# Kernel tuning notes

Measured on AMD Instinct MI355X. Metric: run time of the kernel, lower is better.

The kernel has to match this reference:

```python
import jax, jax.numpy as jnp
import numpy as np

EMB = 256
T = 32          # block_size (hardcoded causal mask length)
HEAD = 128      # total head_size
NH = 8          # n_heads
DH = HEAD // NH # 16 per-head size
B = 4096
EPS = 1e-5


def _ln(x, g, b):
    mu = jnp.mean(x, -1, keepdims=True)
    var = jnp.var(x, -1, keepdims=True)
    return (x - mu) * jax.lax.rsqrt(var + EPS) * g + b


def setup_inputs() -> dict:
    key = jax.random.key(0)
    ks = jax.random.split(key, 12)
    s_in = 1.0 / np.sqrt(EMB)
    s_h = 1.0 / np.sqrt(HEAD)
    s_ff = 1.0 / np.sqrt(4 * EMB)
    return {
        "X": jax.random.normal(ks[0], (B, T, EMB), jnp.float32),
        "ln_g": jnp.ones((EMB,), jnp.float32),
        "ln_b": jnp.zeros((EMB,), jnp.float32),
        # per-head Q/K/V projections packed: [EMB, HEAD] == concat of NH [EMB, DH] heads
        "Wq": jax.random.uniform(ks[1], (EMB, HEAD), jnp.float32, -s_in, s_in),
        "bq": jax.random.uniform(ks[2], (HEAD,), jnp.float32, -s_in, s_in),
        "Wk": jax.random.uniform(ks[3], (EMB, HEAD), jnp.float32, -s_in, s_in),
        "bk": jax.random.uniform(ks[4], (HEAD,), jnp.float32, -s_in, s_in),
        "Wv": jax.random.uniform(ks[5], (EMB, HEAD), jnp.float32, -s_in, s_in),
        "bv": jax.random.uniform(ks[6], (HEAD,), jnp.float32, -s_in, s_in),
        "Wo": jax.random.uniform(ks[7], (HEAD, EMB), jnp.float32, -s_h, s_h),
        "bo": jax.random.uniform(ks[8], (EMB,), jnp.float32, -s_h, s_h),
        "W1": jax.random.uniform(ks[9], (EMB, 4 * EMB), jnp.float32, -s_in, s_in),
        "b1": jax.random.uniform(ks[10], (4 * EMB,), jnp.float32, -s_in, s_in),
        "W2": jax.random.uniform(ks[11], (4 * EMB, EMB), jnp.float32, -s_ff, s_ff),
        "b2": jax.random.uniform(jax.random.fold_in(key, 99), (EMB,), jnp.float32, -s_ff, s_ff),
    }


def reference(X, ln_g, ln_b, Wq, bq, Wk, bk, Wv, bv, Wo, bo, W1, b1, W2, b2):
    h = _ln(X, ln_g, ln_b)                              # [B,T,E]
    # packed QKV, split into heads: [B,T,NH,DH]
    Q = (h @ Wq + bq).reshape(B, T, NH, DH)
    K = (h @ Wk + bk).reshape(B, T, NH, DH)
    V = (h @ Wv + bv).reshape(B, T, NH, DH)
    scores = jnp.einsum("bqhd,bkhd->bhqk", Q, K)        # [B,NH,T,T]
    mask = jnp.tril(jnp.ones((T, T), bool))
    # original: masked_fill(-inf) then divide by sqrt(dh); -inf unchanged
    scores = jnp.where(mask, scores / np.sqrt(DH), -jnp.inf)
    attn = jax.nn.softmax(scores, -1)
    ctx = jnp.einsum("bhqk,bkhd->bqhd", attn, V).reshape(B, T, HEAD)
    X = ctx @ Wo + bo + X                               # residual 1
    h2 = _ln(X, ln_g, ln_b)                             # shared LN params
    out = jax.nn.relu(h2 @ W1 + b1) @ W2 + b2 + X       # residual 2
    return out
```

## Files before the change

### kernel.cpp

```cpp
#include <hip/hip_runtime.h>
#include <math.h>

typedef __attribute__((ext_vector_type(8))) __bf16 bf16x8;
typedef __attribute__((ext_vector_type(8))) unsigned short u16x8;
typedef __attribute__((ext_vector_type(4))) unsigned short u16x4;
typedef __attribute__((ext_vector_type(4))) float f32x4;

namespace {
constexpr int EMB = 256;
constexpr int HD  = 128;
constexpr int FF  = 1024;
constexpr float EPSV = 1e-5f;

constexpr int WS_QKV = 0;
constexpr int WS_O   = 98304;
constexpr int WS_1   = 131072;
constexpr int WS_2   = 393216;

__device__ __forceinline__ unsigned short f32_to_bf16(float f) {
    return __builtin_bit_cast(unsigned short, (__bf16)f);
}
__device__ __forceinline__ float bf16_to_f32(unsigned short h) {
    return __builtin_bit_cast(float, ((unsigned int)h) << 16);
}
__device__ __forceinline__ f32x4 mfma16(u16x8 a, u16x8 b, f32x4 c) {
    return __builtin_amdgcn_mfma_f32_16x16x32_bf16(
        __builtin_bit_cast(bf16x8, a), __builtin_bit_cast(bf16x8, b), c, 0, 0, 0);
}
__device__ __forceinline__ int swzB(int row) { return (row & 7) << 4; }

__device__ __forceinline__ u16x8 ldsA256(const unsigned short* base, int row, int k0) {
    int byte = (row * 256 + k0 * 2) ^ swzB(row);
    return *(const u16x8*)((const char*)base + byte);
}
__device__ __forceinline__ u16x8 ldsA512(const unsigned short* base, int row, int k0) {
    int byte = (row * 512 + k0 * 2) ^ swzB(row);
    return *(const u16x8*)((const char*)base + byte);
}
__device__ __forceinline__ u16x8 ldgF(const unsigned short* base, int frag, int lane) {
    return *(const u16x8*)(base + ((size_t)frag * 64 + lane) * 8);
}
}

__global__ __launch_bounds__(256) void wconv(
    const float* __restrict__ Wq, const float* __restrict__ Wk, const float* __restrict__ Wv,
    const float* __restrict__ Wo, const float* __restrict__ W1, const float* __restrict__ W2,
    unsigned short* __restrict__ ws) {
    int e = blockIdx.x * 256 + threadIdx.x;
    int j, lane, kk, nt, n, k;
    float v;
    if (e < WS_O) {
        int t = e; j = t & 7; lane = (t >> 3) & 63; int r2 = t >> 9;
        kk = r2 & 7; nt = r2 >> 3;
        n = nt * 16 + (lane & 15); k = kk * 32 + (lane >> 4) * 8 + j;
        const float* W = (n < 128) ? Wq : ((n < 256) ? Wk : Wv);
        v = W[k * HD + (n & 127)];
    } else if (e < WS_1) {
        int t = e - WS_O; j = t & 7; lane = (t >> 3) & 63; int r2 = t >> 9;
        kk = r2 & 3; nt = r2 >> 2;
        n = nt * 16 + (lane & 15); k = kk * 32 + (lane >> 4) * 8 + j;
        v = Wo[k * EMB + n];
    } else if (e < WS_2) {
        int t = e - WS_1; j = t & 7; lane = (t >> 3) & 63; int r2 = t >> 9;
        kk = r2 & 7; nt = r2 >> 3;
        n = nt * 16 + (lane & 15); k = kk * 32 + (lane >> 4) * 8 + j;
        v = W1[k * FF + n];
    } else {
        int t = e - WS_2; j = t & 7; lane = (t >> 3) & 63; int r2 = t >> 9;
        kk = r2 & 31; nt = r2 >> 5;
        n = nt * 16 + (lane & 15); k = kk * 32 + (lane >> 4) * 8 + j;
        v = W2[k * EMB + n];
    }
    ws[e] = f32_to_bf16(v);
}

__global__ __launch_bounds__(256, 2) void attn_part(
    const float* __restrict__ X, const float* __restrict__ ln_g, const float* __restrict__ ln_b,
    const float* __restrict__ bq, const float* __restrict__ bk, const float* __restrict__ bv,
    const float* __restrict__ bo, const unsigned short* __restrict__ ws,
    float* __restrict__ x1out) {
    __shared__ __attribute__((aligned(16))) char smem[40960];
    unsigned short* hb = (unsigned short*)smem;
    unsigned short* Qb = (unsigned short*)(smem + 16384);
    char* Kc           = smem + 24576;
    char* Vc           = smem + 32768;

    const unsigned short* WTqkv = ws + WS_QKV;
    const unsigned short* WTo   = ws + WS_O;

    const int tid  = threadIdx.x;
    const int wv   = tid >> 6;
    const int mh   = wv & 1;
    const int nh   = wv >> 1;
    const int lane = tid & 63;
    const int lr   = lane & 15;
    const int lh   = lane >> 4;
    const int row0 = blockIdx.x * 32;
    const f32x4 Z  = {0.f, 0.f, 0.f, 0.f};

    {
        const int r = tid >> 3, sub = tid & 7;
        const float* xr = X + (size_t)(row0 + r) * EMB;
        float4 vv[8];
        float s = 0.f, ss = 0.f;
        #pragma unroll
        for (int j = 0; j < 8; ++j) {
            float4 v = *(const float4*)&xr[sub * 4 + j * 32];
            vv[j] = v;
            s  += (v.x + v.y) + (v.z + v.w);
            ss += (v.x * v.x + v.y * v.y) + (v.z * v.z + v.w * v.w);
        }
        #pragma unroll
        for (int w = 1; w < 8; w <<= 1) { s += __shfl_xor(s, w, 64); ss += __shfl_xor(ss, w, 64); }
        float mu  = s * (1.f / EMB);
        float inv = rsqrtf(fmaxf(ss * (1.f / EMB) - mu * mu, 0.f) + EPSV);
        #pragma unroll
        for (int j = 0; j < 8; ++j) {
            int c = sub * 4 + j * 32;
            float4 v = vv[j];
            float4 g4 = *(const float4*)&ln_g[c];
            float4 b4 = *(const float4*)&ln_b[c];
            u16x4 pk;
            pk[0] = f32_to_bf16((v.x - mu) * inv * g4.x + b4.x);
            pk[1] = f32_to_bf16((v.y - mu) * inv * g4.y + b4.y);
            pk[2] = f32_to_bf16((v.z - mu) * inv * g4.z + b4.z);
            pk[3] = f32_to_bf16((v.w - mu) * inv * g4.w + b4.w);
            *(u16x4*)((char*)hb + ((r * 512 + c * 2) ^ swzB(r))) = pk;
        }
    }
    __syncthreads();

    {
        u16x8 afr[8];
        #pragma unroll
        for (int kk = 0; kk < 8; ++kk)
            afr[kk] = ldsA512(hb, mh * 16 + lr, kk * 32 + lh * 8);
        #pragma unroll 1
        for (int i = 0; i < 12; ++i) {
            int nt = nh * 12 + i;
            u16x8 bfr[8];
            #pragma unroll
            for (int kk = 0; kk < 8; ++kk) bfr[kk] = ldgF(WTqkv, nt * 8 + kk, lane);
            f32x4 e = Z, o = Z;
            #pragma unroll
            for (int kk = 0; kk < 8; kk += 2) {
                e = mfma16(afr[kk], bfr[kk], e);
                o = mfma16(afr[kk + 1], bfr[kk + 1], o);
            }
            f32x4 a = e + o;
            int gcol = nt * 16 + lr;
            int mat = gcol >> 7, c = gcol & 127;
            const float* bias = (mat == 0) ? bq : ((mat == 1) ? bk : bv);
            float bc = bias[c];
            char* regbase = smem + 16384 + mat * 8192;
            #pragma unroll
            for (int reg = 0; reg < 4; ++reg) {
                int r0 = mh * 16 + lh * 4 + reg;
                *(unsigned short*)(regbase + ((r0 * 256 + c * 2) ^ swzB(r0))) =
                    f32_to_bf16(a[reg] + bc);
            }
        }
    }
    __syncthreads();

    {
        const int hd = tid >> 5, q = tid & 31;
        int by0 = (q * 256 + hd * 32) ^ swzB(q);
        int by1 = (q * 256 + hd * 32 + 16) ^ swzB(q);
        float qreg[16];
        {
            u16x8 a = *(const u16x8*)((const char*)Qb + by0);
            u16x8 b_ = *(const u16x8*)((const char*)Qb + by1);
            #pragma unroll
            for (int j = 0; j < 8; ++j) { qreg[j] = bf16_to_f32(a[j]); qreg[8 + j] = bf16_to_f32(b_[j]); }
        }
        float mmax = -1e30f;
        #pragma unroll 4
        for (int k = 0; k < 32; ++k) {
            int kb0 = (k * 256 + hd * 32) ^ swzB(k);
            int kb1 = (k * 256 + hd * 32 + 16) ^ swzB(k);
            u16x8 a = *(const u16x8*)(Kc + kb0);
            u16x8 b_ = *(const u16x8*)(Kc + kb1);
            float s_ = 0.f;
            #pragma unroll
            for (int j = 0; j < 8; ++j)
                s_ += qreg[j] * bf16_to_f32(a[j]) + qreg[8 + j] * bf16_to_f32(b_[j]);
            s_ *= 0.25f;
            if (k <= q) mmax = fmaxf(mmax, s_);
        }
        float den = 0.f;
        float ctx[16];
        #pragma unroll
        for (int j = 0; j < 16; ++j) ctx[j] = 0.f;
        #pragma unroll 4
        for (int k = 0; k < 32; ++k) {
            int kb0 = (k * 256 + hd * 32) ^ swzB(k);
            int kb1 = (k * 256 + hd * 32 + 16) ^ swzB(k);
            u16x8 a = *(const u16x8*)(Kc + kb0);
            u16x8 b_ = *(const u16x8*)(Kc + kb1);
            float s_ = 0.f;
            #pragma unroll
            for (int j = 0; j < 8; ++j)
                s_ += qreg[j] * bf16_to_f32(a[j]) + qreg[8 + j] * bf16_to_f32(b_[j]);
            s_ *= 0.25f;
            float e = (k <= q) ? __expf(s_ - mmax) : 0.f;
            den += e;
            u16x8 va = *(const u16x8*)(Vc + kb0);
            u16x8 vb = *(const u16x8*)(Vc + kb1);
            #pragma unroll
            for (int j = 0; j < 8; ++j) { ctx[j] += e * bf16_to_f32(va[j]); ctx[8 + j] += e * bf16_to_f32(vb[j]); }
        }
        float rd = 1.f / den;
        u16x8 o0, o1;
        #pragma unroll
        for (int j = 0; j < 8; ++j) { o0[j] = f32_to_bf16(ctx[j] * rd); o1[j] = f32_to_bf16(ctx[8 + j] * rd); }
        *(u16x8*)((char*)Qb + by0) = o0;
        *(u16x8*)((char*)Qb + by1) = o1;
    }
    __syncthreads();

    {
        u16x8 afr[4];
        #pragma unroll
        for (int kk = 0; kk < 4; ++kk)
            afr[kk] = ldsA256(Qb, mh * 16 + lr, kk * 32 + lh * 8);
        #pragma unroll 1
        for (int i = 0; i < 8; ++i) {
            int nt = nh * 8 + i;
            u16x8 bfr[4];
            #pragma unroll
            for (int kk = 0; kk < 4; ++kk) bfr[kk] = ldgF(WTo, nt * 4 + kk, lane);
            int col = nt * 16 + lr;
            float bc = bo[col];
            f32x4 e = Z, o = Z;
            e = mfma16(afr[0], bfr[0], e);
            o = mfma16(afr[1], bfr[1], o);
            e = mfma16(afr[2], bfr[2], e);
            o = mfma16(afr[3], bfr[3], o);
            f32x4 a = e + o;
            #pragma unroll
            for (int reg = 0; reg < 4; ++reg) {
                int r0 = mh * 16 + lh * 4 + reg;
                size_t gi = (size_t)(row0 + r0) * EMB + col;
                x1out[gi] = a[reg] + bc + X[gi];
            }
        }
    }
}

__global__ __launch_bounds__(256, 2) void ffn_part(
    const float* __restrict__ ln_g, const float* __restrict__ ln_b,
    const float* __restrict__ b1, const float* __restrict__ b2,
    const unsigned short* __restrict__ ws, float* __restrict__ io) {
    __shared__ __attribute__((aligned(16))) char smem[24576];
    unsigned short* h2  = (unsigned short*)smem;
    unsigned short* fch = (unsigned short*)(smem + 16384);

    const unsigned short* WT1 = ws + WS_1;
    const unsigned short* WT2 = ws + WS_2;

    const int tid  = threadIdx.x;
    const int wv   = tid >> 6;
    const int lane = tid & 63;
    const int lr   = lane & 15;
    const int lh   = lane >> 4;
    const int row0 = blockIdx.x * 32;
    const f32x4 Z  = {0.f, 0.f, 0.f, 0.f};

    {
        const int r = tid >> 3, sub = tid & 7;
        const float* xr = io + (size_t)(row0 + r) * EMB;
        float4 vv[8];
        float s = 0.f, ss = 0.f;
        #pragma unroll
        for (int j = 0; j < 8; ++j) {
            float4 v = *(const float4*)&xr[sub * 4 + j * 32];
            vv[j] = v;
            s  += (v.x + v.y) + (v.z + v.w);
            ss += (v.x * v.x + v.y * v.y) + (v.z * v.z + v.w * v.w);
        }
        #pragma unroll
        for (int w = 1; w < 8; w <<= 1) { s += __shfl_xor(s, w, 64); ss += __shfl_xor(ss, w, 64); }
        float mu  = s * (1.f / EMB);
        float inv = rsqrtf(fmaxf(ss * (1.f / EMB) - mu * mu, 0.f) + EPSV);
        #pragma unroll
        for (int j = 0; j < 8; ++j) {
            int c = sub * 4 + j * 32;
            float4 v = vv[j];
            float4 g4 = *(const float4*)&ln_g[c];
            float4 b4 = *(const float4*)&ln_b[c];
            u16x4 pk;
            pk[0] = f32_to_bf16((v.x - mu) * inv * g4.x + b4.x);
            pk[1] = f32_to_bf16((v.y - mu) * inv * g4.y + b4.y);
            pk[2] = f32_to_bf16((v.z - mu) * inv * g4.z + b4.z);
            pk[3] = f32_to_bf16((v.w - mu) * inv * g4.w + b4.w);
            *(u16x4*)((char*)h2 + ((r * 512 + c * 2) ^ swzB(r))) = pk;
        }
    }
    __syncthreads();

    {
        f32x4 acc2[2][4];
        #pragma unroll
        for (int mt = 0; mt < 2; ++mt)
            #pragma unroll
            for (int i = 0; i < 4; ++i) acc2[mt][i] = Z;

        #pragma unroll 1
        for (int ch = 0; ch < 8; ++ch) {
            #pragma unroll
            for (int f = 0; f < 2; ++f) {
                int fn = ch * 8 + wv * 2 + f;
                u16x8 bAll[8];
                #pragma unroll
                for (int kk = 0; kk < 8; ++kk) bAll[kk] = ldgF(WT1, fn * 8 + kk, lane);
                float bc = b1[fn * 16 + lr];
                int cc = (wv * 2 + f) * 16 + lr;
                #pragma unroll 1
                for (int mt = 0; mt < 2; ++mt) {
                    u16x8 afr[8];
                    #pragma unroll
                    for (int kk = 0; kk < 8; ++kk)
                        afr[kk] = ldsA512(h2, mt * 16 + lr, kk * 32 + lh * 8);
                    f32x4 e = Z, o = Z;
                    #pragma unroll
                    for (int kk = 0; kk < 8; kk += 2) {
                        e = mfma16(afr[kk], bAll[kk], e);
                        o = mfma16(afr[kk + 1], bAll[kk + 1], o);
                    }
                    f32x4 a = e + o;
                    #pragma unroll
                    for (int reg = 0; reg < 4; ++reg) {
                        int r0 = mt * 16 + lh * 4 + reg;
                        *(unsigned short*)((char*)fch + ((r0 * 256 + cc * 2) ^ swzB(r0))) =
                            f32_to_bf16(fmaxf(a[reg] + bc, 0.f));
                    }
                }
            }
            __syncthreads();
            {
                u16x8 afr2[2][4];
                #pragma unroll
                for (int mt = 0; mt < 2; ++mt)
                    #pragma unroll
                    for (int kk = 0; kk < 4; ++kk)
                        afr2[mt][kk] = ldsA256(fch, mt * 16 + lr, kk * 32 + lh * 8);
                #pragma unroll 1
                for (int i = 0; i < 4; ++i) {
                    u16x8 b2f[4];
                    #pragma unroll
                    for (int kk = 0; kk < 4; ++kk)
                        b2f[kk] = ldgF(WT2, (wv * 4 + i) * 32 + ch * 4 + kk, lane);
                    f32x4 t0 = acc2[0][i];
                    t0 = mfma16(afr2[0][0], b2f[0], t0);
                    t0 = mfma16(afr2[0][1], b2f[1], t0);
                    t0 = mfma16(afr2[0][2], b2f[2], t0);
                    t0 = mfma16(afr2[0][3], b2f[3], t0);
                    acc2[0][i] = t0;
                    f32x4 t1 = acc2[1][i];
                    t1 = mfma16(afr2[1][0], b2f[0], t1);
                    t1 = mfma16(afr2[1][1], b2f[1], t1);
                    t1 = mfma16(afr2[1][2], b2f[2], t1);
                    t1 = mfma16(afr2[1][3], b2f[3], t1);
                    acc2[1][i] = t1;
                }
            }
            __syncthreads();
        }
        #pragma unroll
        for (int i = 0; i < 4; ++i) {
            int col = (wv * 4 + i) * 16 + lr;
            float bc = b2[col];
            #pragma unroll
            for (int mt = 0; mt < 2; ++mt) {
                #pragma unroll
                for (int reg = 0; reg < 4; ++reg) {
                    int r0 = mt * 16 + lh * 4 + reg;
                    size_t gi = (size_t)(row0 + r0) * EMB + col;
                    io[gi] = acc2[mt][i][reg] + bc + io[gi];
                }
            }
        }
    }
}

extern "C" void kernel_launch(void* const* d_in, const int* in_sizes, int n_in,
                              void* d_out, int out_size, void* d_ws, size_t ws_size,
                              hipStream_t stream) {
    const float* X    = (const float*)d_in[0];
    const float* ln_g = (const float*)d_in[1];
    const float* ln_b = (const float*)d_in[2];
    const float* Wq   = (const float*)d_in[3];
    const float* bq   = (const float*)d_in[4];
    const float* Wk   = (const float*)d_in[5];
    const float* bk   = (const float*)d_in[6];
    const float* Wv   = (const float*)d_in[7];
    const float* bv   = (const float*)d_in[8];
    const float* Wo   = (const float*)d_in[9];
    const float* bo   = (const float*)d_in[10];
    const float* W1   = (const float*)d_in[11];
    const float* b1   = (const float*)d_in[12];
    const float* W2   = (const float*)d_in[13];
    const float* b2   = (const float*)d_in[14];
    unsigned short* ws = (unsigned short*)d_ws;
    float* O = (float*)d_out;

    wconv<<<2560, 256, 0, stream>>>(Wq, Wk, Wv, Wo, W1, W2, ws);
    attn_part<<<4096, 256, 0, stream>>>(X, ln_g, ln_b, bq, bk, bv, bo, ws, O);
    ffn_part<<<4096, 256, 0, stream>>>(ln_g, ln_b, b1, b2, ws, O);
}
```

Measured before the change: 387.1 us.

## Process 64 rows per FFN block with 8 waves to double weight reuse

The FFN kernel now handles 64 token rows per block with 512 threads instead of 32 rows with 256 threads, and shared memory grows to hold the larger LayerNorm and hidden-activation tiles. Each wave computes one 16-column slice of the W1 chunk across four M-tiles, then two output column tiles of W2 across four M-tiles. Each W1/W2 fragment fetched from global memory is therefore reused across twice as many rows, halving weight traffic per row. In exchange, there are fewer, larger blocks, more accumulator registers per wave, and the launch bounds are relaxed to a 512-thread block with a minimum of one block per CU.

```diff
diff --git a/kernel.cpp b/kernel.cpp
--- a/kernel.cpp
+++ b/kernel.cpp
@@ -248,13 +248,13 @@
     }
 }
 
-__global__ __launch_bounds__(256, 2) void ffn_part(
+__global__ __launch_bounds__(512, 1) void ffn_part(
     const float* __restrict__ ln_g, const float* __restrict__ ln_b,
     const float* __restrict__ b1, const float* __restrict__ b2,
     const unsigned short* __restrict__ ws, float* __restrict__ io) {
-    __shared__ __attribute__((aligned(16))) char smem[24576];
+    __shared__ __attribute__((aligned(16))) char smem[49152];
     unsigned short* h2  = (unsigned short*)smem;
-    unsigned short* fch = (unsigned short*)(smem + 16384);
+    unsigned short* fch = (unsigned short*)(smem + 32768);
 
     const unsigned short* WT1 = ws + WS_1;
     const unsigned short* WT2 = ws + WS_2;
@@ -264,7 +264,7 @@
     const int lane = tid & 63;
     const int lr   = lane & 15;
     const int lh   = lane >> 4;
-    const int row0 = blockIdx.x * 32;
+    const int row0 = blockIdx.x * 64;
     const f32x4 Z  = {0.f, 0.f, 0.f, 0.f};
 
     {
@@ -300,24 +300,21 @@
     __syncthreads();
 
     {
-        f32x4 acc2[2][4];
-        #pragma unroll
-        for (int mt = 0; mt < 2; ++mt)
-            #pragma unroll
-            for (int i = 0; i < 4; ++i) acc2[mt][i] = Z;
+        f32x4 acc2[4][2];
+        #pragma unroll
+        for (int mt = 0; mt < 4; ++mt) { acc2[mt][0] = Z; acc2[mt][1] = Z; }
 
         #pragma unroll 1
         for (int ch = 0; ch < 8; ++ch) {
-            #pragma unroll
-            for (int f = 0; f < 2; ++f) {
-                int fn = ch * 8 + wv * 2 + f;
+            {
+                int fn = ch * 8 + wv;
                 u16x8 bAll[8];
                 #pragma unroll
                 for (int kk = 0; kk < 8; ++kk) bAll[kk] = ldgF(WT1, fn * 8 + kk, lane);
                 float bc = b1[fn * 16 + lr];
-                int cc = (wv * 2 + f) * 16 + lr;
+                int cc = wv * 16 + lr;
                 #pragma unroll 1
-                for (int mt = 0; mt < 2; ++mt) {
+                for (int mt = 0; mt < 4; ++mt) {
                     u16x8 afr[8];
                     #pragma unroll
                     for (int kk = 0; kk < 8; ++kk)
@@ -338,41 +335,34 @@
                 }
             }
             __syncthreads();
-            {
-                u16x8 afr2[2][4];
+            #pragma unroll
+            for (int i = 0; i < 2; ++i) {
+                u16x8 b2f[4];
                 #pragma unroll
-                for (int mt = 0; mt < 2; ++mt)
+                for (int kk = 0; kk < 4; ++kk)
+                    b2f[kk] = ldgF(WT2, (wv * 2 + i) * 32 + ch * 4 + kk, lane);
+                #pragma unroll
+                for (int mt = 0; mt < 4; ++mt) {
+                    u16x8 afr2[4];
                     #pragma unroll
                     for (int kk = 0; kk < 4; ++kk)
-                        afr2[mt][kk] = ldsA256(fch, mt * 16 + lr, kk * 32 + lh * 8);
-                #pragma unroll 1
-                for (int i = 0; i < 4; ++i) {
-                    u16x8 b2f[4];
-                    #pragma unroll
-                    for (int kk = 0; kk < 4; ++kk)
-                        b2f[kk] = ldgF(WT2, (wv * 4 + i) * 32 + ch * 4 + kk, lane);
-                    f32x4 t0 = acc2[0][i];
-                    t0 = mfma16(afr2[0][0], b2f[0], t0);
-                    t0 = mfma16(afr2[0][1], b2f[1], t0);
-                    t0 = mfma16(afr2[0][2], b2f[2], t0);
-                    t0 = mfma16(afr2[0][3], b2f[3], t0);
-                    acc2[0][i] = t0;
-                    f32x4 t1 = acc2[1][i];
-                    t1 = mfma16(afr2[1][0], b2f[0], t1);
-                    t1 = mfma16(afr2[1][1], b2f[1], t1);
-                    t1 = mfma16(afr2[1][2], b2f[2], t1);
-                    t1 = mfma16(afr2[1][3], b2f[3], t1);
-                    acc2[1][i] = t1;
+                        afr2[kk] = ldsA256(fch, mt * 16 + lr, kk * 32 + lh * 8);
+                    f32x4 t = acc2[mt][i];
+                    t = mfma16(afr2[0], b2f[0], t);
+                    t = mfma16(afr2[1], b2f[1], t);
+                    t = mfma16(afr2[2], b2f[2], t);
+                    t = mfma16(afr2[3], b2f[3], t);
+                    acc2[mt][i] = t;
                 }
             }
             __syncthreads();
         }
         #pragma unroll
-        for (int i = 0; i < 4; ++i) {
-            int col = (wv * 4 + i) * 16 + lr;
+        for (int i = 0; i < 2; ++i) {
+            int col = (wv * 2 + i) * 16 + lr;
             float bc = b2[col];
             #pragma unroll
-            for (int mt = 0; mt < 2; ++mt) {
+            for (int mt = 0; mt < 4; ++mt) {
                 #pragma unroll
                 for (int reg = 0; reg < 4; ++reg) {
                     int r0 = mt * 16 + lh * 4 + reg;
@@ -407,5 +397,5 @@
 
     wconv<<<2560, 256, 0, stream>>>(Wq, Wk, Wv, Wo, W1, W2, ws);
     attn_part<<<4096, 256, 0, stream>>>(X, ln_g, ln_b, bq, bk, bv, bo, ws, O);
-    ffn_part<<<4096, 256, 0, stream>>>(ln_g, ln_b, b1, b2, ws, O);
-}
+    ffn_part<<<2048, 512, 0, stream>>>(ln_g, ln_b, b1, b2, ws, O);
+}
```

After: 353.9 us. -8.6%, faster.
